# Optimization experiments

Hardware: AMD Instinct MI355X
Metric: run time of the kernel (lower is better)

Reference implementation:

```python
import jax, jax.numpy as jnp
import numpy as np

N = 100000
E = 1600000
D_IN = 128
D_HID = 128
D_OUT = 128


def _glorot(key, shape):
    fan_in, fan_out = shape[1], shape[0]
    lim = np.sqrt(6.0 / (fan_in + fan_out)).astype(np.float32)
    return jax.random.uniform(key, shape, jnp.float32, -lim, lim)


def setup_inputs() -> dict:
    key = jax.random.key(0)
    ks = jax.random.split(key, 8)
    x = jax.random.normal(ks[0], (N, D_IN), jnp.float32)
    edge_index = jax.random.randint(ks[1], (2, E), 0, N, jnp.int64)
    # SAGEConv params: lin_l acts on aggregated neighbors (has bias), lin_r on root.
    W1l = _glorot(ks[2], (D_HID, D_IN))
    W1r = _glorot(ks[3], (D_HID, D_IN))
    b1 = jnp.zeros((D_HID,), jnp.float32)
    W2l = _glorot(ks[4], (D_OUT, D_HID))
    W2r = _glorot(ks[5], (D_OUT, D_HID))
    b2 = jnp.zeros((D_OUT,), jnp.float32)
    return {"x": x, "edge_index": edge_index,
            "W1l": W1l, "W1r": W1r, "b1": b1,
            "W2l": W2l, "W2r": W2r, "b2": b2}


def _sage_conv(x, src, dst, Wl, Wr, b):
    # mean-aggregate neighbor features j->i, then lin_l(mean) + lin_r(x) + b
    msgs = x[src]                                             # [E, d]
    summed = jax.ops.segment_sum(msgs, dst, num_segments=N)   # [N, d]
    deg = jax.ops.segment_sum(jnp.ones((src.shape[0],), x.dtype), dst,
                              num_segments=N)                 # [N]
    mean = summed / jnp.maximum(deg, 1.0)[:, None]
    return mean @ Wl.T + x @ Wr.T + b


def reference(x, edge_index, W1l, W1r, b1, W2l, W2r, b2):
    src, dst = edge_index[0], edge_index[1]
    h = jax.nn.relu(_sage_conv(x, src, dst, W1l, W1r, b1))
    # dropout p=0.2 is identity in eval mode
    out = _sage_conv(h, src, dst, W2l, W2r, b2)
    return out
```

## Files before the change

kernel.cpp:

```cpp
#include <hip/hip_runtime.h>
#include <hip/hip_bf16.h>

#define N_NODES 100000
#define N_EDGES 1600000
#define D 128
#define NBUCK 782
#define BSTRIDE 2560
#define EPB 4096
#define G1_TILES 1563
#define SC_BLOCKS ((N_EDGES + EPB - 1) / EPB)

typedef __attribute__((ext_vector_type(8))) short short8v;
typedef __attribute__((ext_vector_type(4))) float f32x4;

__device__ __forceinline__ unsigned short f2bf(float f) {
    unsigned int u = __float_as_uint(f);
    unsigned int r = (u + 0x7fffu + ((u >> 16) & 1u)) >> 16;
    return (unsigned short)r;
}
__device__ __forceinline__ float bf2f(unsigned int lo16) {
    return __uint_as_float(lo16 << 16);
}
__device__ __forceinline__ short8v zero8() {
    short8v z = {0, 0, 0, 0, 0, 0, 0, 0};
    return z;
}
__device__ __forceinline__ short8v cvt8(const float4 p0, const float4 p1) {
    union { __hip_bfloat162 h[4]; short8v s; } u;
    u.h[0] = __float22bfloat162_rn(make_float2(p0.x, p0.y));
    u.h[1] = __float22bfloat162_rn(make_float2(p0.z, p0.w));
    u.h[2] = __float22bfloat162_rn(make_float2(p1.x, p1.y));
    u.h[3] = __float22bfloat162_rn(make_float2(p1.z, p1.w));
    return u.s;
}

__global__ __launch_bounds__(256) void k_fused1(
    const float* __restrict__ Af,
    const float* __restrict__ W1l, const float* __restrict__ W1r,
    const float* __restrict__ bias,
    unsigned short* __restrict__ Tout,
    unsigned short* __restrict__ Hout,
    const int* __restrict__ src, const int* __restrict__ dst,
    int* __restrict__ gcnt, unsigned int* __restrict__ ebuf)
{
    if (blockIdx.x >= G1_TILES) {
        __shared__ int cnt[NBUCK];
        __shared__ int base[NBUCK];
        const int t = threadIdx.x;
        const int e0 = (blockIdx.x - G1_TILES) * EPB;
        for (int i = t; i < NBUCK; i += 256) cnt[i] = 0;
        __syncthreads();
#pragma unroll
        for (int u = 0; u < EPB / 256; ++u) {
            int e = e0 + u * 256 + t;
            if (e < N_EDGES) atomicAdd(&cnt[dst[e] >> 7], 1);
        }
        __syncthreads();
        for (int i = t; i < NBUCK; i += 256) {
            int c = cnt[i];
            base[i] = c ? atomicAdd(&gcnt[i], c) : 0;
            cnt[i] = 0;
        }
        __syncthreads();
#pragma unroll
        for (int u = 0; u < EPB / 256; ++u) {
            int e = e0 + u * 256 + t;
            if (e < N_EDGES) {
                int d = dst[e];
                int b = d >> 7;
                int pos = b * BSTRIDE + base[b] + atomicAdd(&cnt[b], 1);
                ebuf[pos] = ((unsigned int)(d & 127) << 17) | (unsigned int)src[e];
            }
        }
        return;
    }

    const int wid = threadIdx.x >> 6;
    const int lane = threadIdx.x & 63;
    const int l15 = lane & 15, lg = lane >> 4;
    const int col_base = wid * 64;

    short8v bfrag[4][4];
#pragma unroll
    for (int cg = 0; cg < 4; ++cg) {
        const int row = col_base + cg * 16 + l15;
        const float* wrow = (row < 128) ? &W1l[(size_t)row * 128]
                                        : &W1r[(size_t)(row - 128) * 128];
#pragma unroll
        for (int ks = 0; ks < 4; ++ks) {
            const int k0 = ks * 32 + lg * 8;
            bfrag[cg][ks] = cvt8(*(const float4*)&wrow[k0],
                                 *(const float4*)&wrow[k0 + 4]);
        }
    }
    float bv[4];
#pragma unroll
    for (int cg = 0; cg < 4; ++cg)
        bv[cg] = (wid >= 2) ? bias[(wid - 2) * 64 + cg * 16 + l15] : 0.0f;

    const int row0 = blockIdx.x * 64;
    f32x4 acc[4][4];
#pragma unroll
    for (int rg = 0; rg < 4; ++rg)
#pragma unroll
        for (int cg = 0; cg < 4; ++cg)
            acc[rg][cg] = (f32x4){0.f, 0.f, 0.f, 0.f};

#pragma unroll
    for (int rg = 0; rg < 4; ++rg) {
        const int arow = row0 + rg * 16 + l15;
        short8v afrag[4];
        if (arow < N_NODES) {
#pragma unroll
            for (int ks = 0; ks < 4; ++ks)
                afrag[ks] = cvt8(*(const float4*)&Af[(size_t)arow * 128 + ks * 32 + lg * 8],
                                 *(const float4*)&Af[(size_t)arow * 128 + ks * 32 + lg * 8 + 4]);
        } else {
#pragma unroll
            for (int ks = 0; ks < 4; ++ks) afrag[ks] = zero8();
        }
#pragma unroll
        for (int cg = 0; cg < 4; ++cg)
#pragma unroll
            for (int ks = 0; ks < 4; ++ks)
                acc[rg][cg] = __builtin_amdgcn_mfma_f32_16x16x32_bf16(
                    afrag[ks], bfrag[cg][ks], acc[rg][cg], 0, 0, 0);
    }

    unsigned short* outp = (wid < 2) ? Tout : Hout;
    const int cb = (wid < 2) ? col_base : col_base - 128;
    const bool addb = (wid >= 2);
#pragma unroll
    for (int rg = 0; rg < 4; ++rg) {
        const int rbase = row0 + rg * 16 + lg * 4;
#pragma unroll
        for (int cg = 0; cg < 4; ++cg) {
            const int col = cb + cg * 16 + l15;
#pragma unroll
            for (int i = 0; i < 4; ++i) {
                int row = rbase + i;
                if (row < N_NODES) {
                    float v = acc[rg][cg][i] + (addb ? bv[cg] : 0.0f);
                    *(__hip_bfloat16*)&outp[(size_t)row * 128 + col] = __float2bfloat16(v);
                }
            }
        }
    }
}

__global__ __launch_bounds__(256) void k_bsort(const unsigned int* __restrict__ ebuf,
                                               const int* __restrict__ gcnt,
                                               int* __restrict__ row_start,
                                               int* __restrict__ ssrc) {
    __shared__ int h[128];
    __shared__ int sc[128];
    const int b = blockIdx.x;
    const int t = threadIdx.x;
    const int eb = b * BSTRIDE;
    const int n = gcnt[b];
    if (t < 128) h[t] = 0;
    __syncthreads();
    for (int e = t; e < n; e += 256)
        atomicAdd(&h[ebuf[eb + e] >> 17], 1);
    __syncthreads();
    if (t < 128) sc[t] = h[t];
    __syncthreads();
    for (int o = 1; o < 128; o <<= 1) {
        int add = 0;
        if (t < 128 && t >= o) add = sc[t - o];
        __syncthreads();
        if (t < 128) sc[t] += add;
        __syncthreads();
    }
    if (t < 128) {
        int excl = sc[t] - h[t];
        row_start[b * 129 + t] = eb + excl;
        h[t] = excl;
    }
    if (t == 0) row_start[b * 129 + 128] = eb + n;
    __syncthreads();
    for (int e = t; e < n; e += 256) {
        unsigned int pk = ebuf[eb + e];
        int dl = pk >> 17;
        int pos = eb + atomicAdd(&h[dl], 1);
        ssrc[pos] = (int)(pk & 0x1ffffu);
    }
}

__global__ __launch_bounds__(256) void k_gemm2(
    const unsigned short* __restrict__ M,
    const unsigned short* __restrict__ H,
    const float* __restrict__ W2l, const float* __restrict__ W2r,
    const float* __restrict__ bias,
    float* __restrict__ out)
{
    const int wid = threadIdx.x >> 6;
    const int lane = threadIdx.x & 63;
    const int l15 = lane & 15, lg = lane >> 4;
    const int col_base = wid * 32;

    short8v bfrag[2][8];
#pragma unroll
    for (int cg = 0; cg < 2; ++cg) {
        const int o = col_base + cg * 16 + l15;
        const float* wl = &W2l[(size_t)o * 128];
        const float* wr = &W2r[(size_t)o * 128];
#pragma unroll
        for (int ks = 0; ks < 4; ++ks) {
            const int k0 = ks * 32 + lg * 8;
            bfrag[cg][ks]     = cvt8(*(const float4*)&wl[k0], *(const float4*)&wl[k0 + 4]);
            bfrag[cg][ks + 4] = cvt8(*(const float4*)&wr[k0], *(const float4*)&wr[k0 + 4]);
        }
    }
    float bv[2];
#pragma unroll
    for (int cg = 0; cg < 2; ++cg)
        bv[cg] = bias[col_base + cg * 16 + l15];

    const int row0 = blockIdx.x * 64;
    f32x4 acc[4][2];
#pragma unroll
    for (int rg = 0; rg < 4; ++rg)
#pragma unroll
        for (int cg = 0; cg < 2; ++cg)
            acc[rg][cg] = (f32x4){0.f, 0.f, 0.f, 0.f};

#pragma unroll
    for (int rg = 0; rg < 4; ++rg) {
        const int arow = row0 + rg * 16 + l15;
        short8v afrag[8];
        if (arow < N_NODES) {
#pragma unroll
            for (int ks = 0; ks < 4; ++ks) {
                afrag[ks]     = *(const short8v*)&M[(size_t)arow * 128 + ks * 32 + lg * 8];
                afrag[ks + 4] = *(const short8v*)&H[(size_t)arow * 128 + ks * 32 + lg * 8];
            }
        } else {
#pragma unroll
            for (int ks = 0; ks < 8; ++ks) afrag[ks] = zero8();
        }
#pragma unroll
        for (int cg = 0; cg < 2; ++cg)
#pragma unroll
            for (int ks = 0; ks < 8; ++ks)
                acc[rg][cg] = __builtin_amdgcn_mfma_f32_16x16x32_bf16(
                    afrag[ks], bfrag[cg][ks], acc[rg][cg], 0, 0, 0);
    }

#pragma unroll
    for (int rg = 0; rg < 4; ++rg) {
        const int rbase = row0 + rg * 16 + lg * 4;
#pragma unroll
        for (int cg = 0; cg < 2; ++cg) {
            const int col = col_base + cg * 16 + l15;
#pragma unroll
            for (int i = 0; i < 4; ++i) {
                int row = rbase + i;
                if (row < N_NODES)
                    out[(size_t)row * 128 + col] = acc[rg][cg][i] + bv[cg];
            }
        }
    }
}

template <bool RMW>
__global__ __launch_bounds__(256) void k_agg(
    const unsigned short* __restrict__ t_mat,
    const int* __restrict__ ssrc,
    const int* __restrict__ row_start,
    unsigned short* __restrict__ io)
{
    int w = (blockIdx.x * blockDim.x + threadIdx.x) >> 6;
    int lane = threadIdx.x & 63;
    if (w >= N_NODES) return;
    const int b = w >> 7, dl = w & 127;
    const int rs = row_start[b * 129 + dl];
    const int re = row_start[b * 129 + dl + 1];
    const int d = re - rs;
    const int half = lane >> 5;
    const int l31 = lane & 31;

    uint2 cur;
    cur.x = 0u; cur.y = 0u;
    if (RMW && lane < 32)
        cur = *((const uint2*)io + (size_t)w * 32 + l31);

    const uint2* tlane = (const uint2*)t_mat + l31;
    float a0 = 0.f, a1 = 0.f, a2 = 0.f, a3 = 0.f;

    for (int q0 = rs; q0 < re; q0 += 64) {
        int nb = 0;
        if (q0 + lane < re) nb = ssrc[q0 + lane];
        const int m = min(64, re - q0);
        int q = 0;
        for (; q + 16 <= m; q += 16) {
            uint2 v[8];
#pragma unroll
            for (int u = 0; u < 8; ++u) {
                int j = __shfl(nb, q + u * 2 + half);
                v[u] = tlane[(size_t)j * 32];
            }
#pragma unroll
            for (int u = 0; u < 8; ++u) {
                a0 += bf2f(v[u].x & 0xffffu);
                a1 += __uint_as_float(v[u].x & 0xffff0000u);
                a2 += bf2f(v[u].y & 0xffffu);
                a3 += __uint_as_float(v[u].y & 0xffff0000u);
            }
        }
        for (; q + 2 <= m; q += 2) {
            int j = __shfl(nb, q + half);
            uint2 vv = tlane[(size_t)j * 32];
            a0 += bf2f(vv.x & 0xffffu);
            a1 += __uint_as_float(vv.x & 0xffff0000u);
            a2 += bf2f(vv.y & 0xffffu);
            a3 += __uint_as_float(vv.y & 0xffff0000u);
        }
        if (q < m) {
            int j = __shfl(nb, q);
            if (half == 0) {
                uint2 vv = tlane[(size_t)j * 32];
                a0 += bf2f(vv.x & 0xffffu);
                a1 += __uint_as_float(vv.x & 0xffff0000u);
                a2 += bf2f(vv.y & 0xffffu);
                a3 += __uint_as_float(vv.y & 0xffff0000u);
            }
        }
    }

    a0 += __shfl_xor(a0, 32);
    a1 += __shfl_xor(a1, 32);
    a2 += __shfl_xor(a2, 32);
    a3 += __shfl_xor(a3, 32);

    if (lane < 32) {
        const float inv = 1.0f / (float)max(d, 1);
        float r0, r1, r2, r3;
        if (RMW) {
            r0 = fmaxf(bf2f(cur.x & 0xffffu) + inv * a0, 0.f);
            r1 = fmaxf(__uint_as_float(cur.x & 0xffff0000u) + inv * a1, 0.f);
            r2 = fmaxf(bf2f(cur.y & 0xffffu) + inv * a2, 0.f);
            r3 = fmaxf(__uint_as_float(cur.y & 0xffff0000u) + inv * a3, 0.f);
        } else {
            r0 = inv * a0; r1 = inv * a1; r2 = inv * a2; r3 = inv * a3;
        }
        uint2 o;
        o.x = (unsigned int)f2bf(r0) | ((unsigned int)f2bf(r1) << 16);
        o.y = (unsigned int)f2bf(r2) | ((unsigned int)f2bf(r3) << 16);
        *((uint2*)io + (size_t)w * 32 + l31) = o;
    }
}


extern "C" void kernel_launch(void* const* d_in, const int* in_sizes, int n_in,
                              void* d_out, int out_size, void* d_ws, size_t ws_size,
                              hipStream_t stream) {
    const float* x   = (const float*)d_in[0];
    const int*   ei  = (const int*)d_in[1];
    const float* W1l = (const float*)d_in[2];
    const float* W1r = (const float*)d_in[3];
    const float* b1  = (const float*)d_in[4];
    const float* W2l = (const float*)d_in[5];
    const float* W2r = (const float*)d_in[6];
    const float* b2  = (const float*)d_in[7];
    float* out = (float*)d_out;

    const int* src = ei;
    const int* dst = ei + N_EDGES;

    char* p = (char*)d_ws;
    auto alloc = [&](size_t bytes) {
        char* r = p;
        p += (bytes + 255) & ~(size_t)255;
        return r;
    };
    unsigned short* tb = (unsigned short*)alloc((size_t)N_NODES * D * 2);
    unsigned short* hx = (unsigned short*)alloc((size_t)N_NODES * D * 2);
    unsigned int*   ebuf = (unsigned int*)alloc((size_t)NBUCK * BSTRIDE * 4);
    int*   ssrc      = (int*)alloc((size_t)NBUCK * BSTRIDE * 4);
    int*   gcnt      = (int*)alloc(NBUCK * sizeof(int));
    int*   row_start = (int*)alloc((size_t)NBUCK * 129 * sizeof(int));

    hipMemsetAsync(gcnt, 0, NBUCK * sizeof(int), stream);
    k_fused1<<<G1_TILES + SC_BLOCKS, 256, 0, stream>>>(x, W1l, W1r, b1, tb, hx,
                                                       src, dst, gcnt, ebuf);
    k_bsort<<<NBUCK, 256, 0, stream>>>(ebuf, gcnt, row_start, ssrc);

    const int agg_grid = (N_NODES + 3) / 4;

    k_agg<true><<<agg_grid, 256, 0, stream>>>(tb, ssrc, row_start, hx);

    k_agg<false><<<agg_grid, 256, 0, stream>>>(hx, ssrc, row_start, tb);
    k_gemm2<<<G1_TILES, 256, 0, stream>>>(tb, hx, W2l, W2r, b2, out);
}
```

Measured before the change: 271.1 us.

## Split fused GEMM/bucket-scatter kernel and cache edge payloads in registers during bucketing

The first-layer GEMM is split out of the fused kernel and becomes its own launch, leaving the bucket scatter as a standalone kernel. Both the scatter and the per-bucket sort now read each edge once, record its local atomic rank and payload in registers, and write it after the prefix/base step. This removes the second global read pass over dst/src and ebuf and the second round of shared atomics. The cost is an extra kernel launch, the loss of the overlap between GEMM and scatter, and higher register use from holding 16 or 10 payloads per thread.

```diff
diff --git a/kernel.cpp b/kernel.cpp
--- a/kernel.cpp
+++ b/kernel.cpp
@@ -7,8 +7,6 @@
 #define NBUCK 782
 #define BSTRIDE 2560
 #define EPB 4096
-#define G1_TILES 1563
-#define SC_BLOCKS ((N_EDGES + EPB - 1) / EPB)
 
 typedef __attribute__((ext_vector_type(8))) short short8v;
 typedef __attribute__((ext_vector_type(4))) float f32x4;
@@ -34,116 +32,41 @@
     return u.s;
 }
 
-__global__ __launch_bounds__(256) void k_fused1(
-    const float* __restrict__ Af,
-    const float* __restrict__ W1l, const float* __restrict__ W1r,
-    const float* __restrict__ bias,
-    unsigned short* __restrict__ Tout,
-    unsigned short* __restrict__ Hout,
-    const int* __restrict__ src, const int* __restrict__ dst,
-    int* __restrict__ gcnt, unsigned int* __restrict__ ebuf)
-{
-    if (blockIdx.x >= G1_TILES) {
-        __shared__ int cnt[NBUCK];
-        __shared__ int base[NBUCK];
-        const int t = threadIdx.x;
-        const int e0 = (blockIdx.x - G1_TILES) * EPB;
-        for (int i = t; i < NBUCK; i += 256) cnt[i] = 0;
-        __syncthreads();
-#pragma unroll
-        for (int u = 0; u < EPB / 256; ++u) {
-            int e = e0 + u * 256 + t;
-            if (e < N_EDGES) atomicAdd(&cnt[dst[e] >> 7], 1);
-        }
-        __syncthreads();
-        for (int i = t; i < NBUCK; i += 256) {
-            int c = cnt[i];
-            base[i] = c ? atomicAdd(&gcnt[i], c) : 0;
-            cnt[i] = 0;
-        }
-        __syncthreads();
-#pragma unroll
-        for (int u = 0; u < EPB / 256; ++u) {
-            int e = e0 + u * 256 + t;
-            if (e < N_EDGES) {
-                int d = dst[e];
-                int b = d >> 7;
-                int pos = b * BSTRIDE + base[b] + atomicAdd(&cnt[b], 1);
-                ebuf[pos] = ((unsigned int)(d & 127) << 17) | (unsigned int)src[e];
-            }
-        }
-        return;
-    }
-
-    const int wid = threadIdx.x >> 6;
-    const int lane = threadIdx.x & 63;
-    const int l15 = lane & 15, lg = lane >> 4;
-    const int col_base = wid * 64;
-
-    short8v bfrag[4][4];
-#pragma unroll
-    for (int cg = 0; cg < 4; ++cg) {
-        const int row = col_base + cg * 16 + l15;
-        const float* wrow = (row < 128) ? &W1l[(size_t)row * 128]
-                                        : &W1r[(size_t)(row - 128) * 128];
-#pragma unroll
-        for (int ks = 0; ks < 4; ++ks) {
-            const int k0 = ks * 32 + lg * 8;
-            bfrag[cg][ks] = cvt8(*(const float4*)&wrow[k0],
-                                 *(const float4*)&wrow[k0 + 4]);
-        }
-    }
-    float bv[4];
-#pragma unroll
-    for (int cg = 0; cg < 4; ++cg)
-        bv[cg] = (wid >= 2) ? bias[(wid - 2) * 64 + cg * 16 + l15] : 0.0f;
-
-    const int row0 = blockIdx.x * 64;
-    f32x4 acc[4][4];
-#pragma unroll
-    for (int rg = 0; rg < 4; ++rg)
-#pragma unroll
-        for (int cg = 0; cg < 4; ++cg)
-            acc[rg][cg] = (f32x4){0.f, 0.f, 0.f, 0.f};
-
-#pragma unroll
-    for (int rg = 0; rg < 4; ++rg) {
-        const int arow = row0 + rg * 16 + l15;
-        short8v afrag[4];
-        if (arow < N_NODES) {
-#pragma unroll
-            for (int ks = 0; ks < 4; ++ks)
-                afrag[ks] = cvt8(*(const float4*)&Af[(size_t)arow * 128 + ks * 32 + lg * 8],
-                                 *(const float4*)&Af[(size_t)arow * 128 + ks * 32 + lg * 8 + 4]);
-        } else {
-#pragma unroll
-            for (int ks = 0; ks < 4; ++ks) afrag[ks] = zero8();
-        }
-#pragma unroll
-        for (int cg = 0; cg < 4; ++cg)
-#pragma unroll
-            for (int ks = 0; ks < 4; ++ks)
-                acc[rg][cg] = __builtin_amdgcn_mfma_f32_16x16x32_bf16(
-                    afrag[ks], bfrag[cg][ks], acc[rg][cg], 0, 0, 0);
-    }
-
-    unsigned short* outp = (wid < 2) ? Tout : Hout;
-    const int cb = (wid < 2) ? col_base : col_base - 128;
-    const bool addb = (wid >= 2);
-#pragma unroll
-    for (int rg = 0; rg < 4; ++rg) {
-        const int rbase = row0 + rg * 16 + lg * 4;
-#pragma unroll
-        for (int cg = 0; cg < 4; ++cg) {
-            const int col = cb + cg * 16 + l15;
-#pragma unroll
-            for (int i = 0; i < 4; ++i) {
-                int row = rbase + i;
-                if (row < N_NODES) {
-                    float v = acc[rg][cg][i] + (addb ? bv[cg] : 0.0f);
-                    *(__hip_bfloat16*)&outp[(size_t)row * 128 + col] = __float2bfloat16(v);
-                }
-            }
+__global__ __launch_bounds__(256) void k_bscatter(const int* __restrict__ src,
+                                                  const int* __restrict__ dst,
+                                                  int* __restrict__ gcnt,
+                                                  unsigned int* __restrict__ ebuf) {
+    __shared__ int cnt[NBUCK];
+    __shared__ int base[NBUCK];
+    const int t = threadIdx.x;
+    const int e0 = blockIdx.x * EPB;
+    for (int i = t; i < NBUCK; i += 256) cnt[i] = 0;
+    __syncthreads();
+    unsigned int pay[16];
+    int meta[16];
+#pragma unroll
+    for (int u = 0; u < 16; ++u) {
+        int e = e0 + u * 256 + t;
+        if (e < N_EDGES) {
+            int d = dst[e];
+            int b = d >> 7;
+            int r = atomicAdd(&cnt[b], 1);
+            meta[u] = (b << 16) | r;
+            pay[u] = ((unsigned int)(d & 127) << 17) | (unsigned int)src[e];
+        } else meta[u] = -1;
+    }
+    __syncthreads();
+    for (int i = t; i < NBUCK; i += 256) {
+        int c = cnt[i];
+        base[i] = c ? atomicAdd(&gcnt[i], c) : 0;
+    }
+    __syncthreads();
+#pragma unroll
+    for (int u = 0; u < 16; ++u) {
+        if (meta[u] >= 0) {
+            int b = meta[u] >> 16;
+            int r = meta[u] & 0xffff;
+            ebuf[b * BSTRIDE + base[b] + r] = pay[u];
         }
     }
 }
@@ -160,8 +83,19 @@
     const int n = gcnt[b];
     if (t < 128) h[t] = 0;
     __syncthreads();
-    for (int e = t; e < n; e += 256)
-        atomicAdd(&h[ebuf[eb + e] >> 17], 1);
+    unsigned int pay[BSTRIDE / 256];
+    int meta[BSTRIDE / 256];
+#pragma unroll
+    for (int u = 0; u < BSTRIDE / 256; ++u) {
+        int e = t + u * 256;
+        if (e < n) {
+            unsigned int pk = ebuf[eb + e];
+            int dl = pk >> 17;
+            int r = atomicAdd(&h[dl], 1);
+            meta[u] = (dl << 16) | r;
+            pay[u] = pk;
+        } else meta[u] = -1;
+    }
     __syncthreads();
     if (t < 128) sc[t] = h[t];
     __syncthreads();
@@ -175,15 +109,97 @@
     if (t < 128) {
         int excl = sc[t] - h[t];
         row_start[b * 129 + t] = eb + excl;
-        h[t] = excl;
+        sc[t] = excl;
     }
     if (t == 0) row_start[b * 129 + 128] = eb + n;
     __syncthreads();
-    for (int e = t; e < n; e += 256) {
-        unsigned int pk = ebuf[eb + e];
-        int dl = pk >> 17;
-        int pos = eb + atomicAdd(&h[dl], 1);
-        ssrc[pos] = (int)(pk & 0x1ffffu);
+#pragma unroll
+    for (int u = 0; u < BSTRIDE / 256; ++u) {
+        if (meta[u] >= 0) {
+            int dl = meta[u] >> 16;
+            int r = meta[u] & 0xffff;
+            ssrc[eb + sc[dl] + r] = (int)(pay[u] & 0x1ffffu);
+        }
+    }
+}
+
+__global__ __launch_bounds__(256) void k_gemm1(
+    const float* __restrict__ Af,
+    const float* __restrict__ W1l, const float* __restrict__ W1r,
+    const float* __restrict__ bias,
+    unsigned short* __restrict__ Tout,
+    unsigned short* __restrict__ Hout)
+{
+    const int wid = threadIdx.x >> 6;
+    const int lane = threadIdx.x & 63;
+    const int l15 = lane & 15, lg = lane >> 4;
+    const int col_base = wid * 64;
+
+    short8v bfrag[4][4];
+#pragma unroll
+    for (int cg = 0; cg < 4; ++cg) {
+        const int row = col_base + cg * 16 + l15;
+        const float* wrow = (row < 128) ? &W1l[(size_t)row * 128]
+                                        : &W1r[(size_t)(row - 128) * 128];
+#pragma unroll
+        for (int ks = 0; ks < 4; ++ks) {
+            const int k0 = ks * 32 + lg * 8;
+            bfrag[cg][ks] = cvt8(*(const float4*)&wrow[k0],
+                                 *(const float4*)&wrow[k0 + 4]);
+        }
+    }
+    float bv[4];
+#pragma unroll
+    for (int cg = 0; cg < 4; ++cg)
+        bv[cg] = (wid >= 2) ? bias[(wid - 2) * 64 + cg * 16 + l15] : 0.0f;
+
+    const int row0 = blockIdx.x * 64;
+    f32x4 acc[4][4];
+#pragma unroll
+    for (int rg = 0; rg < 4; ++rg)
+#pragma unroll
+        for (int cg = 0; cg < 4; ++cg)
+            acc[rg][cg] = (f32x4){0.f, 0.f, 0.f, 0.f};
+
+#pragma unroll
+    for (int rg = 0; rg < 4; ++rg) {
+        const int arow = row0 + rg * 16 + l15;
+        short8v afrag[4];
+        if (arow < N_NODES) {
+#pragma unroll
+            for (int ks = 0; ks < 4; ++ks)
+                afrag[ks] = cvt8(*(const float4*)&Af[(size_t)arow * 128 + ks * 32 + lg * 8],
+                                 *(const float4*)&Af[(size_t)arow * 128 + ks * 32 + lg * 8 + 4]);
+        } else {
+#pragma unroll
+            for (int ks = 0; ks < 4; ++ks) afrag[ks] = zero8();
+        }
+#pragma unroll
+        for (int cg = 0; cg < 4; ++cg)
+#pragma unroll
+            for (int ks = 0; ks < 4; ++ks)
+                acc[rg][cg] = __builtin_amdgcn_mfma_f32_16x16x32_bf16(
+                    afrag[ks], bfrag[cg][ks], acc[rg][cg], 0, 0, 0);
+    }
+
+    unsigned short* outp = (wid < 2) ? Tout : Hout;
+    const int cb = (wid < 2) ? col_base : col_base - 128;
+    const bool addb = (wid >= 2);
+#pragma unroll
+    for (int rg = 0; rg < 4; ++rg) {
+        const int rbase = row0 + rg * 16 + lg * 4;
+#pragma unroll
+        for (int cg = 0; cg < 4; ++cg) {
+            const int col = cb + cg * 16 + l15;
+#pragma unroll
+            for (int i = 0; i < 4; ++i) {
+                int row = rbase + i;
+                if (row < N_NODES) {
+                    float v = acc[rg][cg][i] + (addb ? bv[cg] : 0.0f);
+                    *(__hip_bfloat16*)&outp[(size_t)row * 128 + col] = __float2bfloat16(v);
+                }
+            }
+        }
     }
 }
 
@@ -381,15 +397,16 @@
     int*   gcnt      = (int*)alloc(NBUCK * sizeof(int));
     int*   row_start = (int*)alloc((size_t)NBUCK * 129 * sizeof(int));
 
+    const int g1_tiles = (N_NODES + 63) / 64;
+    const int agg_grid = (N_NODES + 3) / 4;
+
     hipMemsetAsync(gcnt, 0, NBUCK * sizeof(int), stream);
-    k_fused1<<<G1_TILES + SC_BLOCKS, 256, 0, stream>>>(x, W1l, W1r, b1, tb, hx,
-                                                       src, dst, gcnt, ebuf);
+    k_bscatter<<<(N_EDGES + EPB - 1) / EPB, 256, 0, stream>>>(src, dst, gcnt, ebuf);
     k_bsort<<<NBUCK, 256, 0, stream>>>(ebuf, gcnt, row_start, ssrc);
 
-    const int agg_grid = (N_NODES + 3) / 4;
-
+    k_gemm1<<<g1_tiles, 256, 0, stream>>>(x, W1l, W1r, b1, tb, hx);
     k_agg<true><<<agg_grid, 256, 0, stream>>>(tb, ssrc, row_start, hx);
 
     k_agg<false><<<agg_grid, 256, 0, stream>>>(hx, ssrc, row_start, tb);
-    k_gemm2<<<G1_TILES, 256, 0, stream>>>(tb, hx, W2l, W2r, b2, out);
-}
+    k_gemm2<<<g1_tiles, 256, 0, stream>>>(tb, hx, W2l, W2r, b2, out);
+}
```

Result: slower. 283.6 us (+4.6%).
